# Performance work log

Hardware: AMD Instinct MI355X
Metric: run time of the kernel (lower is better)

## Reference

```python
import jax, jax.numpy as jnp
import numpy as np

NUM_BLOCKS = 2
NUM_LAYERS = 10
L = NUM_BLOCKS * NUM_LAYERS  # 20 wave layers
C_IN, C_RES, C_SKIP = 8, 64, 256
B, T = 32, 4096


def causal_conv1d(x, w, b, dilation=1):
    # x: [B, C_in, T], w: [C_out, C_in, K], left-pad so output is causal and length-preserving
    k = w.shape[2]
    out = jax.lax.conv_general_dilated(
        x, w, window_strides=(1,), padding=[(dilation * (k - 1), 0)],
        rhs_dilation=(dilation,), dimension_numbers=("NCH", "OIH", "NCH"))
    return out + b[None, :, None]


def setup_inputs() -> dict:
    key = jax.random.key(0)
    ks = jax.random.split(key, 12)
    s1 = 1.0 / np.sqrt(C_IN)
    s2 = 1.0 / np.sqrt(2 * C_RES)
    s3 = 1.0 / np.sqrt(C_RES)
    return {
        "x":    jax.random.normal(ks[0], (B, C_IN, T), jnp.float32),
        "w_in": jax.random.normal(ks[1], (C_RES, C_IN, 1), jnp.float32) * s1,
        "b_in": jax.random.normal(ks[2], (C_RES,), jnp.float32) * s1,
        "w_f":  jax.random.normal(ks[3], (L, C_RES, C_RES, 2), jnp.float32) * s2,
        "b_f":  jax.random.normal(ks[4], (L, C_RES), jnp.float32) * s2,
        "w_g":  jax.random.normal(ks[5], (L, C_RES, C_RES, 2), jnp.float32) * s2,
        "b_g":  jax.random.normal(ks[6], (L, C_RES), jnp.float32) * s2,
        "w_s":  jax.random.normal(ks[7], (L, C_SKIP, C_RES, 1), jnp.float32) * s3,
        "b_s":  jax.random.normal(ks[8], (L, C_SKIP), jnp.float32) * s3,
        "w_r":  jax.random.normal(ks[9], (L, C_RES, C_RES, 1), jnp.float32) * s3,
        "b_r":  jax.random.normal(ks[10], (L, C_RES), jnp.float32) * s3,
    }


def reference(x, w_in, b_in, w_f, b_f, w_g, b_g, w_s, b_s, w_r, b_r):
    # WaveNet.encode: 1x1 input conv, then num_blocks*num_layers gated dilated causal layers
    h = causal_conv1d(x, w_in, b_in)            # [B, C_RES, T]
    skips = jnp.zeros((x.shape[0], w_s.shape[1], x.shape[2]), x.dtype)
    for i in range(L):
        d = 2 ** (i % NUM_LAYERS)
        f = jnp.tanh(causal_conv1d(h, w_f[i], b_f[i], d))
        g = jax.nn.sigmoid(causal_conv1d(h, w_g[i], b_g[i], d))
        z = f * g                                # gated activation
        skips = skips + causal_conv1d(z, w_s[i], b_s[i])
        h = h + causal_conv1d(z, w_r[i], b_r[i])  # residual connection
    return skips
```

## Files before the change

kernel.cpp:

```cpp
#include <hip/hip_runtime.h>

#define B_ 32
#define T_ 4096
#define CR 64
#define CS 256
#define NL 20

typedef __bf16 bf16x8 __attribute__((ext_vector_type(8)));
typedef __bf16 bf16x4v __attribute__((ext_vector_type(4)));
typedef float f32x4 __attribute__((ext_vector_type(4)));
typedef unsigned int u32x2 __attribute__((ext_vector_type(2)));

__device__ __forceinline__ f32x4 mfma16(bf16x8 a, bf16x8 b, f32x4 c) {
  return __builtin_amdgcn_mfma_f32_16x16x32_bf16(a, b, c, 0, 0, 0);
}

__device__ __forceinline__ void dma16(const __bf16* g, __bf16* l) {
  __builtin_amdgcn_global_load_lds(
      (const __attribute__((address_space(1))) unsigned int*)g,
      (__attribute__((address_space(3))) unsigned int*)l, 16, 0, 0);
}

__global__ void pack_kernel(const float* __restrict__ wf, const float* __restrict__ wg,
                            const float* __restrict__ wsn, const float* __restrict__ wr,
                            const float* __restrict__ bs,
                            __bf16* __restrict__ Wfg2, __bf16* __restrict__ Wr2,
                            __bf16* __restrict__ Ws2, float* __restrict__ bsS) {
  int n = blockIdx.x * 256 + threadIdx.x;
  if (n < 327680) {
    int j = n & 7, lane = (n >> 3) & 63, fr = (n >> 9) & 7, mt = (n >> 12) & 3, i = n >> 14;
    int cs = mt * 16 + (lane & 15);
    int k = (fr & 3) * 32 + (lane >> 4) * 8 + j;
    int ci = k & 63, tap = k >> 6;
    const float* src = (fr < 4) ? wf : wg;
    Wfg2[n] = (__bf16)src[((i * 64 + cs) * 64 + ci) * 2 + tap];
  } else if (n < 409600) {
    int m = n - 327680;
    int j = m & 7, lane = (m >> 3) & 63, kc = (m >> 9) & 1, mt = (m >> 10) & 3, i = m >> 12;
    int cs = mt * 16 + (lane & 15);
    int ci = kc * 32 + (lane >> 4) * 8 + j;
    Wr2[m] = (__bf16)wr[(i * 64 + cs) * 64 + ci];
  } else if (n < 737280) {
    int m = n - 409600;
    int j = m & 7, lane = (m >> 3) & 63, kc = (m >> 9) & 1, tile = (m >> 10) & 15, i = m >> 14;
    int cs = tile * 16 + (lane & 15);
    int ci = kc * 32 + (lane >> 4) * 8 + j;
    Ws2[m] = (__bf16)wsn[i * 16384 + cs * 64 + ci];
  } else if (n < 737536) {
    int cs = n - 737280;
    float s = 0.f;
    for (int i = 0; i < NL; ++i) s += bs[i * 256 + cs];
    bsS[cs] = s;
  }
}

__global__ void inconv_kernel(const float* __restrict__ x, const float* __restrict__ w_in,
                              const float* __restrict__ b_in, float* __restrict__ h0) {
  __shared__ float w[64][8];
  __shared__ float bi[64];
  int tid = threadIdx.x;
  for (int k = tid; k < 512; k += 256) w[k >> 3][k & 7] = w_in[k];
  if (tid < 64) bi[tid] = b_in[tid];
  __syncthreads();
  int b = blockIdx.x >> 4;
  int t = ((blockIdx.x & 15) << 8) + tid;
  float xv[8];
#pragma unroll
  for (int ci = 0; ci < 8; ++ci) xv[ci] = x[((size_t)b * 8 + ci) * T_ + t];
  float* orow = h0 + ((size_t)b * T_ + t) * 64;
#pragma unroll
  for (int c0 = 0; c0 < 64; c0 += 4) {
    float s0 = bi[c0], s1 = bi[c0 + 1], s2 = bi[c0 + 2], s3 = bi[c0 + 3];
#pragma unroll
    for (int ci = 0; ci < 8; ++ci) {
      s0 += w[c0][ci] * xv[ci];
      s1 += w[c0 + 1][ci] * xv[ci];
      s2 += w[c0 + 2][ci] * xv[ci];
      s3 += w[c0 + 3][ci] * xv[ci];
    }
    float4 o = make_float4(s0, s1, s2, s3);
    *(float4*)(orow + c0) = o;
  }
}

__global__ __launch_bounds__(256) void layer_kernel(
    const float* __restrict__ h_in, float* __restrict__ h_out,
    const __bf16* __restrict__ Wfg, const __bf16* __restrict__ Wr,
    const float* __restrict__ bF, const float* __restrict__ bG,
    const float* __restrict__ bR,
    __bf16* __restrict__ Zg, int d, int il, int Gs, int last) {
  __shared__ __bf16 sB[2][64][72];

  const int tid = threadIdx.x;
  const int bid = ((blockIdx.x & 7) << 8) | (blockIdx.x >> 3);
  const int b = bid >> 6;
  const int t0 = (bid & 63) << 6;
  const float* hbase = h_in + ((size_t)b * T_ + t0) * 64;

  float4 vc[4];
#pragma unroll
  for (int it = 0; it < 4; ++it) {
    int f = (it * 256 + tid) * 4;
    vc[it] = *(const float4*)(hbase + f);
  }

  if (d >= 64) {
    float4 vd[4];
#pragma unroll
    for (int it = 0; it < 4; ++it) {
      int f = (it * 256 + tid) * 4;
      int trr = f >> 6, c = f & 63;
      int td = t0 + trr - d;
      vd[it] = make_float4(0.f, 0.f, 0.f, 0.f);
      if (td >= 0) vd[it] = *(const float4*)(h_in + ((size_t)b * T_ + td) * 64 + c);
    }
#pragma unroll
    for (int it = 0; it < 4; ++it) {
      int f = (it * 256 + tid) * 4;
      int trr = f >> 6, c = f & 63;
      bf16x4v pd = {(__bf16)vd[it].x, (__bf16)vd[it].y, (__bf16)vd[it].z, (__bf16)vd[it].w};
      *(bf16x4v*)&sB[0][trr][c] = pd;
    }
  } else {
    for (int f2 = tid; f2 < (d << 4); f2 += 256) {
      int trr = f2 >> 4, c = (f2 & 15) << 2;
      int td = t0 + trr - d;
      float4 u = make_float4(0.f, 0.f, 0.f, 0.f);
      if (td >= 0) u = *(const float4*)(h_in + ((size_t)b * T_ + td) * 64 + c);
      bf16x4v pd = {(__bf16)u.x, (__bf16)u.y, (__bf16)u.z, (__bf16)u.w};
      *(bf16x4v*)&sB[0][trr][c] = pd;
    }
  }

#pragma unroll
  for (int it = 0; it < 4; ++it) {
    int f = (it * 256 + tid) * 4;
    int trr = f >> 6, c = f & 63;
    bf16x4v pc = {(__bf16)vc[it].x, (__bf16)vc[it].y, (__bf16)vc[it].z, (__bf16)vc[it].w};
    *(bf16x4v*)&sB[1][trr][c] = pc;
  }
  __syncthreads();

  const int lane = tid & 63, wid = tid >> 6;
  const int tl = (wid << 4) | (lane & 15);
  const int kq = lane >> 4;

  const __bf16* pdel = (tl < d) ? &sB[0][tl][0] : &sB[1][tl - d][0];
  bf16x8 bh[4];
  bh[0] = *(const bf16x8*)(pdel + kq * 8);
  bh[1] = *(const bf16x8*)(pdel + 32 + kq * 8);
  bh[2] = *(const bf16x8*)&sB[1][tl][kq * 8];
  bh[3] = *(const bf16x8*)&sB[1][tl][32 + kq * 8];

  __bf16 (*sZ)[72] = sB[0];
  __bf16* ztile = Zg + ((size_t)bid * Gs + il) * 4096;

#pragma unroll
  for (int mt = 0; mt < 4; ++mt) {
    const __bf16* wb = Wfg + (mt * 8) * 512 + lane * 8;
    f32x4 aF = {0.f, 0.f, 0.f, 0.f}, aG = {0.f, 0.f, 0.f, 0.f};
#pragma unroll
    for (int kc = 0; kc < 4; ++kc) {
      aF = mfma16(*(const bf16x8*)(wb + kc * 512), bh[kc], aF);
      aG = mfma16(*(const bf16x8*)(wb + (4 + kc) * 512), bh[kc], aG);
    }
    const int c0 = (mt << 4) + (kq << 2);
    float4 bfv = *(const float4*)(bF + c0);
    float4 bgv = *(const float4*)(bG + c0);
    float fb[4] = {bfv.x, bfv.y, bfv.z, bfv.w};
    float gb[4] = {bgv.x, bgv.y, bgv.z, bgv.w};
    bf16x4v zv;
#pragma unroll
    for (int r = 0; r < 4; ++r) {
      float fp = aF[r] + fb[r];
      float gp = aG[r] + gb[r];
      float e = __expf(2.f * fp);
      float th = 1.f - 2.f / (e + 1.f);
      float sg = 1.f / (1.f + __expf(-gp));
      zv[r] = (__bf16)(th * sg);
    }
    *(bf16x4v*)&sZ[tl][c0] = zv;
    {
      const int kc = mt >> 1;
      const int l = ((mt & 1) * 2 + (kq >> 1)) * 16 + (lane & 15);
      const int j0 = (kq & 1) * 4;
      u32x2 zu = __builtin_bit_cast(u32x2, zv);
      __builtin_nontemporal_store(
          zu, (u32x2*)(ztile + (size_t)(wid * 2 + kc) * 512 + l * 8 + j0));
    }
  }

  if (!last) {
    bf16x8 bz0 = *(const bf16x8*)&sZ[tl][kq * 8];
    bf16x8 bz1 = *(const bf16x8*)&sZ[tl][32 + kq * 8];
#pragma unroll
    for (int mt = 0; mt < 4; ++mt) {
      const __bf16* wrb = Wr + (mt * 2) * 512 + lane * 8;
      f32x4 aR = {0.f, 0.f, 0.f, 0.f};
      aR = mfma16(*(const bf16x8*)(wrb), bz0, aR);
      aR = mfma16(*(const bf16x8*)(wrb + 512), bz1, aR);
      const int c0 = (mt << 4) + (kq << 2);
      float4 hv = *(const float4*)(h_in + ((size_t)b * T_ + t0 + tl) * 64 + c0);
      float4 brv = *(const float4*)(bR + c0);
      float4 o;
      o.x = hv.x + aR[0] + brv.x;
      o.y = hv.y + aR[1] + brv.y;
      o.z = hv.z + aR[2] + brv.z;
      o.w = hv.w + aR[3] + brv.w;
      *(float4*)(h_out + ((size_t)b * T_ + t0 + tl) * 64 + c0) = o;
    }
  }
}

__global__ __launch_bounds__(256) void skip_kernel(
    const __bf16* __restrict__ Zg, const __bf16* __restrict__ Ws2,
    const float* __restrict__ bsS, float* __restrict__ out,
    int i0, int cnt, int Gs, int first) {
  __shared__ __bf16 sZ[3][4096];

  const int tid = threadIdx.x;
  const int b = blockIdx.x >> 6;
  const int t0 = (blockIdx.x & 63) << 6;
  const int lane = tid & 63, wid = tid >> 6;
  const int kq = lane >> 4;

  const __bf16* ztile = Zg + ((size_t)blockIdx.x * Gs + i0) * 4096;
  const __bf16* wbase = Ws2 + (size_t)i0 * 16384 + (size_t)(wid * 8) * 512 + lane * 8;
  __bf16* ldsw = &sZ[0][0] + (size_t)(wid * 2) * 512;

#define DMA_TILE(ilx, bufx)                                                   \
  do {                                                                        \
    const __bf16* gsrc_ = ztile + (size_t)(ilx) * 4096 + (wid * 2) * 512 + lane * 8; \
    __bf16* ld_ = ldsw + (size_t)(bufx) * 4096;                               \
    dma16(gsrc_, ld_);                                                        \
    dma16(gsrc_ + 512, ld_ + 512);                                            \
  } while (0)

  f32x4 acc[16];
#pragma unroll
  for (int q = 0; q < 16; ++q) acc[q] = (f32x4){0.f, 0.f, 0.f, 0.f};

  bf16x8 awA[8], awB[8];

  DMA_TILE(0, 0);
  __builtin_amdgcn_sched_barrier(0);
#pragma unroll
  for (int f = 0; f < 8; ++f) awA[f] = *(const bf16x8*)(wbase + f * 512);
  __builtin_amdgcn_sched_barrier(0);
  if (cnt > 1) {
    DMA_TILE(1, 1);
    __builtin_amdgcn_sched_barrier(0);
    asm volatile("s_waitcnt vmcnt(10)" ::: "memory");
  } else {
    __builtin_amdgcn_sched_barrier(0);
    asm volatile("s_waitcnt vmcnt(8)" ::: "memory");
  }
  __builtin_amdgcn_s_barrier();
  __builtin_amdgcn_sched_barrier(0);

#define SKIP_STEP(AWU, AWP)                                                   \
  do {                                                                        \
    const bool have1 = (il + 1) < cnt, have2 = (il + 2) < cnt;                \
    if (have2) {                                                              \
      int b2 = cur + 2;                                                       \
      if (b2 >= 3) b2 -= 3;                                                   \
      DMA_TILE(il + 2, b2);                                                   \
    }                                                                         \
    __builtin_amdgcn_sched_barrier(0);                                        \
    if (have1) {                                                              \
      const __bf16* wn_ = wbase + (size_t)(il + 1) * 16384;                   \
      _Pragma("unroll") for (int f = 0; f < 8; ++f)                           \
          AWP[f] = *(const bf16x8*)(wn_ + f * 512);                           \
    }                                                                         \
    const __bf16* zb_ = &sZ[0][0] + (size_t)cur * 4096 + lane * 8;            \
    bf16x8 bz[4];                                                             \
    _Pragma("unroll") for (int f = 0; f < 4; ++f)                             \
        bz[f] = *(const bf16x8*)(zb_ + f * 512);                              \
    _Pragma("unroll") for (int mt = 0; mt < 4; ++mt)                          \
        _Pragma("unroll") for (int nt = 0; nt < 2; ++nt) {                    \
      acc[mt * 4 + nt] = mfma16(AWU[mt * 2], bz[nt * 2], acc[mt * 4 + nt]);   \
      acc[mt * 4 + nt] = mfma16(AWU[mt * 2 + 1], bz[nt * 2 + 1], acc[mt * 4 + nt]); \
    }                                                                         \
    _Pragma("unroll") for (int f = 0; f < 4; ++f)                             \
        bz[f] = *(const bf16x8*)(zb_ + (4 + f) * 512);                        \
    _Pragma("unroll") for (int mt = 0; mt < 4; ++mt)                          \
        _Pragma("unroll") for (int nt = 0; nt < 2; ++nt) {                    \
      acc[mt * 4 + nt + 2] = mfma16(AWU[mt * 2], bz[nt * 2], acc[mt * 4 + nt + 2]); \
      acc[mt * 4 + nt + 2] =                                                  \
          mfma16(AWU[mt * 2 + 1], bz[nt * 2 + 1], acc[mt * 4 + nt + 2]);      \
    }                                                                         \
    if (have1) {                                                              \
      __builtin_amdgcn_sched_barrier(0);                                      \
      asm volatile("s_waitcnt vmcnt(10) lgkmcnt(0)" ::: "memory");            \
      __builtin_amdgcn_s_barrier();                                           \
      __builtin_amdgcn_sched_barrier(0);                                      \
    }                                                                         \
  } while (0)

  int il = 0, cur = 0;
  while (true) {
    SKIP_STEP(awA, awB);
    if (++il == cnt) break;
    cur = (cur == 2) ? 0 : cur + 1;
    SKIP_STEP(awB, awA);
    if (++il == cnt) break;
    cur = (cur == 2) ? 0 : cur + 1;
  }

  const int csb = wid * 64 + (kq << 2);
  const int tcol = t0 + (lane & 15);
#pragma unroll
  for (int mt = 0; mt < 4; ++mt) {
#pragma unroll
    for (int nt = 0; nt < 4; ++nt) {
#pragma unroll
      for (int r = 0; r < 4; ++r) {
        int cs = csb + mt * 16 + r;
        size_t idx = ((size_t)b * CS + cs) * T_ + tcol + nt * 16;
        float v = acc[mt * 4 + nt][r];
        if (first) __builtin_nontemporal_store(v + bsS[cs], &out[idx]);
        else out[idx] += v;
      }
    }
  }
}

extern "C" void kernel_launch(void* const* d_in, const int* in_sizes, int n_in,
                              void* d_out, int out_size, void* d_ws, size_t ws_size,
                              hipStream_t stream) {
  (void)in_sizes; (void)n_in; (void)out_size;
  const float* x    = (const float*)d_in[0];
  const float* w_in = (const float*)d_in[1];
  const float* b_in = (const float*)d_in[2];
  const float* w_f  = (const float*)d_in[3];
  const float* b_f  = (const float*)d_in[4];
  const float* w_g  = (const float*)d_in[5];
  const float* b_g  = (const float*)d_in[6];
  const float* w_s  = (const float*)d_in[7];
  const float* b_s  = (const float*)d_in[8];
  const float* w_r  = (const float*)d_in[9];
  const float* b_r  = (const float*)d_in[10];
  float* out = (float*)d_out;

  char* ws = (char*)d_ws;
  size_t off = 0;
  auto alloc = [&](size_t bytes) -> char* {
    char* p = ws + off;
    off = (off + bytes + 255) & ~(size_t)255;
    return p;
  };
  float* hA = (float*)alloc((size_t)B_ * T_ * 64 * 4);
  float* hB = (float*)alloc((size_t)B_ * T_ * 64 * 4);
  __bf16* Wfg2 = (__bf16*)alloc((size_t)NL * 16384 * 2);
  __bf16* Wr2  = (__bf16*)alloc((size_t)NL * 4096 * 2);
  __bf16* Ws2  = (__bf16*)alloc((size_t)NL * 16384 * 2);
  float* bsS = (float*)alloc(CS * 4);

  size_t zslot = (size_t)B_ * T_ * 64 * 2;
  size_t rem = (ws_size > off) ? (ws_size - off) : 0;
  int G = (int)(rem / zslot);
  if (G > NL) G = NL;
  if (G < 1) G = 1;
  __bf16* Zg = (__bf16*)(ws + off);

  hipLaunchKernelGGL(pack_kernel, dim3(2881), dim3(256), 0, stream,
                     w_f, w_g, w_s, w_r, b_s, Wfg2, Wr2, Ws2, bsS);
  hipLaunchKernelGGL(inconv_kernel, dim3(512), dim3(256), 0, stream, x, w_in, b_in, hA);

  float* hc = hA;
  float* hn = hB;
  int i0 = 0;
  for (int i = 0; i < NL; ++i) {
    int il = i - i0;
    hipLaunchKernelGGL(layer_kernel, dim3(B_ * 64), dim3(256), 0, stream,
                       hc, hn, Wfg2 + (size_t)i * 16384, Wr2 + (size_t)i * 4096,
                       b_f + i * 64, b_g + i * 64, b_r + i * 64,
                       Zg, 1 << (i % 10), il, G, (i == NL - 1) ? 1 : 0);
    { float* tmp = hc; hc = hn; hn = tmp; }
    if (il + 1 == G || i == NL - 1) {
      int cnt = il + 1;
      hipLaunchKernelGGL(skip_kernel, dim3(B_ * 64), dim3(256), 0, stream,
                         Zg, Ws2, bsS, out, i0, cnt, G, (i0 == 0) ? 1 : 0);
      i0 = i + 1;
    }
  }
}
```

Baseline: 873.8 us.

## Fuse layer launches into persistent kernel with software grid barrier

Replaces the per-layer kernel launches with one persistent kernel per skip group. It uses 512 blocks that each handle four time tiles and separates layers with an atomic-based grid barrier. Within a block, the loads for the next tile are issued before the current tile is computed, so global latency overlaps MFMA work. It also drops the nontemporal store on the first skip write. The barrier needs all 512 blocks resident at once and adds spin and fence costs at every layer.

```diff
diff --git a/kernel.cpp b/kernel.cpp
--- a/kernel.cpp
+++ b/kernel.cpp
@@ -5,6 +5,7 @@
 #define CR 64
 #define CS 256
 #define NL 20
+#define GRID_P 512
 
 typedef __bf16 bf16x8 __attribute__((ext_vector_type(8)));
 typedef __bf16 bf16x4v __attribute__((ext_vector_type(4)));
@@ -21,11 +22,31 @@
       (__attribute__((address_space(3))) unsigned int*)l, 16, 0, 0);
 }
 
+__device__ __forceinline__ void grid_sync(unsigned* bar, unsigned nblk) {
+  __syncthreads();
+  if (threadIdx.x == 0) {
+    __threadfence();
+    unsigned gen = __hip_atomic_load(&bar[1], __ATOMIC_RELAXED, __HIP_MEMORY_SCOPE_AGENT);
+    unsigned old = __hip_atomic_fetch_add(&bar[0], 1u, __ATOMIC_RELAXED, __HIP_MEMORY_SCOPE_AGENT);
+    if (old == nblk - 1) {
+      __hip_atomic_store(&bar[0], 0u, __ATOMIC_RELAXED, __HIP_MEMORY_SCOPE_AGENT);
+      __threadfence();
+      __hip_atomic_fetch_add(&bar[1], 1u, __ATOMIC_RELAXED, __HIP_MEMORY_SCOPE_AGENT);
+    } else {
+      while (__hip_atomic_load(&bar[1], __ATOMIC_RELAXED, __HIP_MEMORY_SCOPE_AGENT) == gen)
+        __builtin_amdgcn_s_sleep(8);
+    }
+    __threadfence();
+  }
+  __syncthreads();
+}
+
 __global__ void pack_kernel(const float* __restrict__ wf, const float* __restrict__ wg,
                             const float* __restrict__ wsn, const float* __restrict__ wr,
                             const float* __restrict__ bs,
                             __bf16* __restrict__ Wfg2, __bf16* __restrict__ Wr2,
-                            __bf16* __restrict__ Ws2, float* __restrict__ bsS) {
+                            __bf16* __restrict__ Ws2, float* __restrict__ bsS,
+                            unsigned* __restrict__ bar) {
   int n = blockIdx.x * 256 + threadIdx.x;
   if (n < 327680) {
     int j = n & 7, lane = (n >> 3) & 63, fr = (n >> 9) & 7, mt = (n >> 12) & 3, i = n >> 14;
@@ -51,6 +72,8 @@
     float s = 0.f;
     for (int i = 0; i < NL; ++i) s += bs[i * 256 + cs];
     bsS[cs] = s;
+  } else if (n < 737538) {
+    bar[n - 737536] = 0u;
   }
 }
 
@@ -83,132 +106,188 @@
   }
 }
 
-__global__ __launch_bounds__(256) void layer_kernel(
-    const float* __restrict__ h_in, float* __restrict__ h_out,
-    const __bf16* __restrict__ Wfg, const __bf16* __restrict__ Wr,
-    const float* __restrict__ bF, const float* __restrict__ bG,
-    const float* __restrict__ bR,
-    __bf16* __restrict__ Zg, int d, int il, int Gs, int last) {
+__global__ __launch_bounds__(256, 2) void layers_kernel(
+    float* h0, float* h1,
+    const __bf16* __restrict__ Wfg2, const __bf16* __restrict__ Wr2,
+    const float* __restrict__ bf0, const float* __restrict__ bg0,
+    const float* __restrict__ br0,
+    __bf16* __restrict__ Zg, unsigned* __restrict__ bar,
+    int i0, int cnt, int Gs, int lastgrp) {
   __shared__ __bf16 sB[2][64][72];
 
   const int tid = threadIdx.x;
-  const int bid = ((blockIdx.x & 7) << 8) | (blockIdx.x >> 3);
-  const int b = bid >> 6;
-  const int t0 = (bid & 63) << 6;
-  const float* hbase = h_in + ((size_t)b * T_ + t0) * 64;
-
-  float4 vc[4];
-#pragma unroll
-  for (int it = 0; it < 4; ++it) {
-    int f = (it * 256 + tid) * 4;
-    vc[it] = *(const float4*)(hbase + f);
-  }
-
-  if (d >= 64) {
-    float4 vd[4];
-#pragma unroll
-    for (int it = 0; it < 4; ++it) {
-      int f = (it * 256 + tid) * 4;
-      int trr = f >> 6, c = f & 63;
-      int td = t0 + trr - d;
-      vd[it] = make_float4(0.f, 0.f, 0.f, 0.f);
-      if (td >= 0) vd[it] = *(const float4*)(h_in + ((size_t)b * T_ + td) * 64 + c);
-    }
-#pragma unroll
-    for (int it = 0; it < 4; ++it) {
-      int f = (it * 256 + tid) * 4;
-      int trr = f >> 6, c = f & 63;
-      bf16x4v pd = {(__bf16)vd[it].x, (__bf16)vd[it].y, (__bf16)vd[it].z, (__bf16)vd[it].w};
-      *(bf16x4v*)&sB[0][trr][c] = pd;
-    }
-  } else {
-    for (int f2 = tid; f2 < (d << 4); f2 += 256) {
-      int trr = f2 >> 4, c = (f2 & 15) << 2;
-      int td = t0 + trr - d;
-      float4 u = make_float4(0.f, 0.f, 0.f, 0.f);
-      if (td >= 0) u = *(const float4*)(h_in + ((size_t)b * T_ + td) * 64 + c);
-      bf16x4v pd = {(__bf16)u.x, (__bf16)u.y, (__bf16)u.z, (__bf16)u.w};
-      *(bf16x4v*)&sB[0][trr][c] = pd;
-    }
-  }
-
-#pragma unroll
-  for (int it = 0; it < 4; ++it) {
-    int f = (it * 256 + tid) * 4;
-    int trr = f >> 6, c = f & 63;
-    bf16x4v pc = {(__bf16)vc[it].x, (__bf16)vc[it].y, (__bf16)vc[it].z, (__bf16)vc[it].w};
-    *(bf16x4v*)&sB[1][trr][c] = pc;
-  }
-  __syncthreads();
-
+  const int sw = ((blockIdx.x & 7) << 6) | (blockIdx.x >> 3);
+  const int b = sw >> 4;
+  const int tb0 = (sw & 15) << 2;
   const int lane = tid & 63, wid = tid >> 6;
   const int tl = (wid << 4) | (lane & 15);
   const int kq = lane >> 4;
 
-  const __bf16* pdel = (tl < d) ? &sB[0][tl][0] : &sB[1][tl - d][0];
-  bf16x8 bh[4];
-  bh[0] = *(const bf16x8*)(pdel + kq * 8);
-  bh[1] = *(const bf16x8*)(pdel + 32 + kq * 8);
-  bh[2] = *(const bf16x8*)&sB[1][tl][kq * 8];
-  bh[3] = *(const bf16x8*)&sB[1][tl][32 + kq * 8];
-
-  __bf16 (*sZ)[72] = sB[0];
-  __bf16* ztile = Zg + ((size_t)bid * Gs + il) * 4096;
-
-#pragma unroll
-  for (int mt = 0; mt < 4; ++mt) {
-    const __bf16* wb = Wfg + (mt * 8) * 512 + lane * 8;
-    f32x4 aF = {0.f, 0.f, 0.f, 0.f}, aG = {0.f, 0.f, 0.f, 0.f};
-#pragma unroll
-    for (int kc = 0; kc < 4; ++kc) {
-      aF = mfma16(*(const bf16x8*)(wb + kc * 512), bh[kc], aF);
-      aG = mfma16(*(const bf16x8*)(wb + (4 + kc) * 512), bh[kc], aG);
-    }
-    const int c0 = (mt << 4) + (kq << 2);
-    float4 bfv = *(const float4*)(bF + c0);
-    float4 bgv = *(const float4*)(bG + c0);
-    float fb[4] = {bfv.x, bfv.y, bfv.z, bfv.w};
-    float gb[4] = {bgv.x, bgv.y, bgv.z, bgv.w};
-    bf16x4v zv;
-#pragma unroll
-    for (int r = 0; r < 4; ++r) {
-      float fp = aF[r] + fb[r];
-      float gp = aG[r] + gb[r];
-      float e = __expf(2.f * fp);
-      float th = 1.f - 2.f / (e + 1.f);
-      float sg = 1.f / (1.f + __expf(-gp));
-      zv[r] = (__bf16)(th * sg);
-    }
-    *(bf16x4v*)&sZ[tl][c0] = zv;
-    {
-      const int kc = mt >> 1;
-      const int l = ((mt & 1) * 2 + (kq >> 1)) * 16 + (lane & 15);
-      const int j0 = (kq & 1) * 4;
-      u32x2 zu = __builtin_bit_cast(u32x2, zv);
-      __builtin_nontemporal_store(
-          zu, (u32x2*)(ztile + (size_t)(wid * 2 + kc) * 512 + l * 8 + j0));
-    }
-  }
-
-  if (!last) {
-    bf16x8 bz0 = *(const bf16x8*)&sZ[tl][kq * 8];
-    bf16x8 bz1 = *(const bf16x8*)&sZ[tl][32 + kq * 8];
-#pragma unroll
-    for (int mt = 0; mt < 4; ++mt) {
-      const __bf16* wrb = Wr + (mt * 2) * 512 + lane * 8;
-      f32x4 aR = {0.f, 0.f, 0.f, 0.f};
-      aR = mfma16(*(const bf16x8*)(wrb), bz0, aR);
-      aR = mfma16(*(const bf16x8*)(wrb + 512), bz1, aR);
-      const int c0 = (mt << 4) + (kq << 2);
-      float4 hv = *(const float4*)(h_in + ((size_t)b * T_ + t0 + tl) * 64 + c0);
-      float4 brv = *(const float4*)(bR + c0);
-      float4 o;
-      o.x = hv.x + aR[0] + brv.x;
-      o.y = hv.y + aR[1] + brv.y;
-      o.z = hv.z + aR[2] + brv.z;
-      o.w = hv.w + aR[3] + brv.w;
-      *(float4*)(h_out + ((size_t)b * T_ + t0 + tl) * 64 + c0) = o;
-    }
+  for (int k = 0; k < cnt; ++k) {
+    const int i = i0 + k;
+    const int d = 1 << (i % 10);
+    const bool dge = (d >= 64);
+    const float* hin = (k & 1) ? h1 : h0;
+    float* hout = (k & 1) ? h0 : h1;
+    const __bf16* Wfg = Wfg2 + (size_t)i * 16384;
+    const __bf16* Wr = Wr2 + (size_t)i * 4096;
+    const float* bF = bf0 + i * 64;
+    const float* bG = bg0 + i * 64;
+    const float* bR = br0 + i * 64;
+    const bool lastres = lastgrp && (k == cnt - 1);
+
+    float4 vcA[4], vdA[4], vcB[4], vdB[4];
+    float4 vmA0, vmA1, vmB0, vmB1;
+
+    auto ISSUE = [&](int S, float4* vc, float4* vd, float4& vm0, float4& vm1) {
+      const int t0_ = (tb0 + S) << 6;
+      const float* hb_ = hin + ((size_t)b * T_ + t0_) * 64;
+#pragma unroll
+      for (int it = 0; it < 4; ++it) vc[it] = *(const float4*)(hb_ + (it * 256 + tid) * 4);
+      if (dge) {
+#pragma unroll
+        for (int it = 0; it < 4; ++it) {
+          int f_ = (it * 256 + tid) * 4;
+          int trr_ = f_ >> 6, c_ = f_ & 63;
+          int td_ = t0_ + trr_ - d;
+          vd[it] = make_float4(0.f, 0.f, 0.f, 0.f);
+          if (td_ >= 0) vd[it] = *(const float4*)(hin + ((size_t)b * T_ + td_) * 64 + c_);
+        }
+      } else {
+        const int nm = d << 4;
+        vm0 = make_float4(0.f, 0.f, 0.f, 0.f);
+        vm1 = make_float4(0.f, 0.f, 0.f, 0.f);
+        if (tid < nm) {
+          int trr_ = tid >> 4, c_ = (tid & 15) << 2;
+          int td_ = t0_ + trr_ - d;
+          if (td_ >= 0) vm0 = *(const float4*)(hin + ((size_t)b * T_ + td_) * 64 + c_);
+        }
+        int f2_ = tid + 256;
+        if (f2_ < nm) {
+          int trr_ = f2_ >> 4, c_ = (f2_ & 15) << 2;
+          int td_ = t0_ + trr_ - d;
+          if (td_ >= 0) vm1 = *(const float4*)(hin + ((size_t)b * T_ + td_) * 64 + c_);
+        }
+      }
+    };
+
+    auto WRITE = [&](float4* vc, float4* vd, float4& vm0, float4& vm1) {
+#pragma unroll
+      for (int it = 0; it < 4; ++it) {
+        int f_ = (it * 256 + tid) * 4;
+        int trr_ = f_ >> 6, c_ = f_ & 63;
+        bf16x4v pc_ = {(__bf16)vc[it].x, (__bf16)vc[it].y, (__bf16)vc[it].z, (__bf16)vc[it].w};
+        *(bf16x4v*)&sB[1][trr_][c_] = pc_;
+      }
+      if (dge) {
+#pragma unroll
+        for (int it = 0; it < 4; ++it) {
+          int f_ = (it * 256 + tid) * 4;
+          int trr_ = f_ >> 6, c_ = f_ & 63;
+          bf16x4v pd_ = {(__bf16)vd[it].x, (__bf16)vd[it].y, (__bf16)vd[it].z, (__bf16)vd[it].w};
+          *(bf16x4v*)&sB[0][trr_][c_] = pd_;
+        }
+      } else {
+        const int nm = d << 4;
+        if (tid < nm) {
+          int trr_ = tid >> 4, c_ = (tid & 15) << 2;
+          bf16x4v pd_ = {(__bf16)vm0.x, (__bf16)vm0.y, (__bf16)vm0.z, (__bf16)vm0.w};
+          *(bf16x4v*)&sB[0][trr_][c_] = pd_;
+        }
+        int f2_ = tid + 256;
+        if (f2_ < nm) {
+          int trr_ = f2_ >> 4, c_ = (f2_ & 15) << 2;
+          bf16x4v pd_ = {(__bf16)vm1.x, (__bf16)vm1.y, (__bf16)vm1.z, (__bf16)vm1.w};
+          *(bf16x4v*)&sB[0][trr_][c_] = pd_;
+        }
+      }
+      __syncthreads();
+    };
+
+    auto COMPUTE = [&](int S, bool dosync) {
+      const int t0_ = (tb0 + S) << 6;
+      const __bf16* pdel = (tl < d) ? &sB[0][tl][0] : &sB[1][tl - d][0];
+      bf16x8 bh[4];
+      bh[0] = *(const bf16x8*)(pdel + kq * 8);
+      bh[1] = *(const bf16x8*)(pdel + 32 + kq * 8);
+      bh[2] = *(const bf16x8*)&sB[1][tl][kq * 8];
+      bh[3] = *(const bf16x8*)&sB[1][tl][32 + kq * 8];
+
+      __bf16(*sZ)[72] = sB[0];
+      __bf16* ztile = Zg + (((size_t)((b << 6) + tb0 + S)) * Gs + k) * 4096;
+
+#pragma unroll
+      for (int mt = 0; mt < 4; ++mt) {
+        const __bf16* wb = Wfg + (mt * 8) * 512 + lane * 8;
+        f32x4 aF = {0.f, 0.f, 0.f, 0.f}, aG = {0.f, 0.f, 0.f, 0.f};
+#pragma unroll
+        for (int kc = 0; kc < 4; ++kc) {
+          aF = mfma16(*(const bf16x8*)(wb + kc * 512), bh[kc], aF);
+          aG = mfma16(*(const bf16x8*)(wb + (4 + kc) * 512), bh[kc], aG);
+        }
+        const int c0 = (mt << 4) + (kq << 2);
+        float4 bfv = *(const float4*)(bF + c0);
+        float4 bgv = *(const float4*)(bG + c0);
+        float fb[4] = {bfv.x, bfv.y, bfv.z, bfv.w};
+        float gb[4] = {bgv.x, bgv.y, bgv.z, bgv.w};
+        bf16x4v zv;
+#pragma unroll
+        for (int r = 0; r < 4; ++r) {
+          float fp = aF[r] + fb[r];
+          float gp = aG[r] + gb[r];
+          float e = __expf(2.f * fp);
+          float th = 1.f - 2.f / (e + 1.f);
+          float sg = 1.f / (1.f + __expf(-gp));
+          zv[r] = (__bf16)(th * sg);
+        }
+        *(bf16x4v*)&sZ[tl][c0] = zv;
+        {
+          const int kc = mt >> 1;
+          const int l = ((mt & 1) * 2 + (kq >> 1)) * 16 + (lane & 15);
+          const int j0 = (kq & 1) * 4;
+          u32x2 zu = __builtin_bit_cast(u32x2, zv);
+          __builtin_nontemporal_store(
+              zu, (u32x2*)(ztile + (size_t)(wid * 2 + kc) * 512 + l * 8 + j0));
+        }
+      }
+
+      if (!lastres) {
+        bf16x8 bz0 = *(const bf16x8*)&sZ[tl][kq * 8];
+        bf16x8 bz1 = *(const bf16x8*)&sZ[tl][32 + kq * 8];
+#pragma unroll
+        for (int mt = 0; mt < 4; ++mt) {
+          const __bf16* wrb = Wr + (mt * 2) * 512 + lane * 8;
+          f32x4 aR = {0.f, 0.f, 0.f, 0.f};
+          aR = mfma16(*(const bf16x8*)(wrb), bz0, aR);
+          aR = mfma16(*(const bf16x8*)(wrb + 512), bz1, aR);
+          const int c0 = (mt << 4) + (kq << 2);
+          float4 hv = *(const float4*)(hin + ((size_t)b * T_ + t0_ + tl) * 64 + c0);
+          float4 brv = *(const float4*)(bR + c0);
+          float4 o;
+          o.x = hv.x + aR[0] + brv.x;
+          o.y = hv.y + aR[1] + brv.y;
+          o.z = hv.z + aR[2] + brv.z;
+          o.w = hv.w + aR[3] + brv.w;
+          *(float4*)(hout + ((size_t)b * T_ + t0_ + tl) * 64 + c0) = o;
+        }
+      }
+      if (dosync) __syncthreads();
+    };
+
+    ISSUE(0, vcA, vdA, vmA0, vmA1);
+    WRITE(vcA, vdA, vmA0, vmA1);
+    ISSUE(1, vcB, vdB, vmB0, vmB1);
+    COMPUTE(0, true);
+    WRITE(vcB, vdB, vmB0, vmB1);
+    ISSUE(2, vcA, vdA, vmA0, vmA1);
+    COMPUTE(1, true);
+    WRITE(vcA, vdA, vmA0, vmA1);
+    ISSUE(3, vcB, vdB, vmB0, vmB1);
+    COMPUTE(2, true);
+    WRITE(vcB, vdB, vmB0, vmB1);
+    COMPUTE(3, false);
+
+    if (k != cnt - 1) grid_sync(bar, GRID_P);
   }
 }
 
@@ -224,7 +303,7 @@
   const int lane = tid & 63, wid = tid >> 6;
   const int kq = lane >> 4;
 
-  const __bf16* ztile = Zg + ((size_t)blockIdx.x * Gs + i0) * 4096;
+  const __bf16* ztile = Zg + ((size_t)blockIdx.x * Gs) * 4096;
   const __bf16* wbase = Ws2 + (size_t)i0 * 16384 + (size_t)(wid * 8) * 512 + lane * 8;
   __bf16* ldsw = &sZ[0][0] + (size_t)(wid * 2) * 512;
 
@@ -318,7 +397,7 @@
         int cs = csb + mt * 16 + r;
         size_t idx = ((size_t)b * CS + cs) * T_ + tcol + nt * 16;
         float v = acc[mt * 4 + nt][r];
-        if (first) __builtin_nontemporal_store(v + bsS[cs], &out[idx]);
+        if (first) out[idx] = v + bsS[cs];
         else out[idx] += v;
       }
     }
@@ -355,6 +434,7 @@
   __bf16* Wr2  = (__bf16*)alloc((size_t)NL * 4096 * 2);
   __bf16* Ws2  = (__bf16*)alloc((size_t)NL * 16384 * 2);
   float* bsS = (float*)alloc(CS * 4);
+  unsigned* bar = (unsigned*)alloc(256);
 
   size_t zslot = (size_t)B_ * T_ * 64 * 2;
   size_t rem = (ws_size > off) ? (ws_size - off) : 0;
@@ -363,25 +443,21 @@
   if (G < 1) G = 1;
   __bf16* Zg = (__bf16*)(ws + off);
 
-  hipLaunchKernelGGL(pack_kernel, dim3(2881), dim3(256), 0, stream,
-                     w_f, w_g, w_s, w_r, b_s, Wfg2, Wr2, Ws2, bsS);
+  hipLaunchKernelGGL(pack_kernel, dim3(2882), dim3(256), 0, stream,
+                     w_f, w_g, w_s, w_r, b_s, Wfg2, Wr2, Ws2, bsS, bar);
   hipLaunchKernelGGL(inconv_kernel, dim3(512), dim3(256), 0, stream, x, w_in, b_in, hA);
 
   float* hc = hA;
   float* hn = hB;
   int i0 = 0;
-  for (int i = 0; i < NL; ++i) {
-    int il = i - i0;
-    hipLaunchKernelGGL(layer_kernel, dim3(B_ * 64), dim3(256), 0, stream,
-                       hc, hn, Wfg2 + (size_t)i * 16384, Wr2 + (size_t)i * 4096,
-                       b_f + i * 64, b_g + i * 64, b_r + i * 64,
-                       Zg, 1 << (i % 10), il, G, (i == NL - 1) ? 1 : 0);
-    { float* tmp = hc; hc = hn; hn = tmp; }
-    if (il + 1 == G || i == NL - 1) {
-      int cnt = il + 1;
-      hipLaunchKernelGGL(skip_kernel, dim3(B_ * 64), dim3(256), 0, stream,
-                         Zg, Ws2, bsS, out, i0, cnt, G, (i0 == 0) ? 1 : 0);
-      i0 = i + 1;
-    }
-  }
-}
+  while (i0 < NL) {
+    int cnt = (G < NL - i0) ? G : (NL - i0);
+    int lastgrp = (i0 + cnt == NL) ? 1 : 0;
+    hipLaunchKernelGGL(layers_kernel, dim3(GRID_P), dim3(256), 0, stream,
+                       hc, hn, Wfg2, Wr2, b_f, b_g, b_r, Zg, bar, i0, cnt, G, lastgrp);
+    if (cnt & 1) { float* tmp = hc; hc = hn; hn = tmp; }
+    hipLaunchKernelGGL(skip_kernel, dim3(B_ * 64), dim3(256), 0, stream,
+                       Zg, Ws2, bsS, out, i0, cnt, G, (i0 == 0) ? 1 : 0);
+    i0 += cnt;
+  }
+}
```

Result: slower. 2.292 ms (+162.3%).
